# Kernel optimization log

Measured on AMD Instinct MI355X. Metric: run time of the kernel, lower is better.

Reference implementation:

```python
import jax, jax.numpy as jnp
import numpy as np

DIM = 768
NUM_HEADS = 8
HEAD_DIM = DIM // NUM_HEADS


def setup_inputs() -> dict:
    key = jax.random.key(0)
    k1, k2, k3, k4, k5 = jax.random.split(key, 5)
    B, C, H, W = 16, DIM, 32, 32
    x = jax.random.normal(k1, (B, C, H, W), dtype=jnp.float32)
    # Conv2d 1x1 weights expressed as [out_ch, in_ch] matrices
    w_qkv = jax.random.normal(k2, (3 * C, C), dtype=jnp.float32) * (C ** -0.5)
    b_qkv = jax.random.normal(k3, (3 * C,), dtype=jnp.float32) * 0.02
    w_proj = jax.random.normal(k4, (C, C), dtype=jnp.float32) * (C ** -0.5)
    b_proj = jax.random.normal(k5, (C,), dtype=jnp.float32) * 0.02
    return {"x": x, "w_qkv": w_qkv, "b_qkv": b_qkv, "w_proj": w_proj, "b_proj": b_proj}


def reference(x, w_qkv, b_qkv, w_proj, b_proj):
    B, C, H, W = x.shape
    N = H * W
    nh, hd = NUM_HEADS, C // NUM_HEADS
    xf = x.astype(jnp.float32).reshape(B, C, N)  # bcn
    # 1x1 conv == channel matmul
    qkv = jnp.einsum('oc,bcn->bon', w_qkv, xf) + b_qkv[None, :, None]
    qkv = qkv.reshape(B, 3, nh, hd, N)
    q, k, v = qkv[:, 0], qkv[:, 1], qkv[:, 2]  # [B, nh, hd, N]
    s = hd ** -0.25  # scale split between q and k as in the original
    attn = jnp.einsum('bhdn,bhdm->bhnm', q * s, k * s)  # [B, nh, N, N]
    attn = attn - jax.lax.stop_gradient(jnp.max(attn, axis=-1, keepdims=True))
    attn = jnp.clip(attn, -88.0, 88.0)
    attn = jax.nn.softmax(attn, axis=-1)
    # dropout is identity in eval mode
    out = jnp.einsum('bhnm,bhdm->bhdn', attn, v)  # [B, nh, hd, N]
    out = out.reshape(B, C, N)
    out = jnp.einsum('oc,bcn->bon', w_proj, out) + b_proj[None, :, None]
    return out.reshape(B, C, H, W).astype(x.dtype)
```

## Files before the change

### kernel.cpp

```cpp
#include <hip/hip_runtime.h>
#include <stdint.h>

typedef __attribute__((ext_vector_type(4))) float f32x4;
typedef __attribute__((ext_vector_type(16))) float f32x16;
typedef __attribute__((ext_vector_type(8))) short bf16x8;

#define SQKV 0.38372606f
#define RM 8.0f

__device__ __forceinline__ unsigned short f2bf(float f) {
  union { float f; unsigned u; } v; v.f = f;
  unsigned r = v.u + 0x7FFFu + ((v.u >> 16) & 1u);
  return (unsigned short)(r >> 16);
}

__device__ __forceinline__ unsigned cvt_pk_bf16(float a, float b) {
  unsigned r;
  asm volatile("v_cvt_pk_bf16_f32 %0, %1, %2" : "=v"(r) : "v"(a), "v"(b));
  return r;
}
__device__ __forceinline__ void permswap(unsigned &a, unsigned &b) {
  asm volatile("v_permlane32_swap_b32 %0, %1" : "+v"(a), "+v"(b));
}

__device__ __forceinline__ void glds16(const unsigned short* g, unsigned short* l) {
  __builtin_amdgcn_global_load_lds(
      (const __attribute__((address_space(1))) void*)g,
      (__attribute__((address_space(3))) void*)l, 16, 0, 0);
}

__global__ __launch_bounds__(256) void k_convert2(const float* __restrict__ s1,
                                                  const float* __restrict__ s2,
                                                  unsigned short* __restrict__ d1,
                                                  int n1_4, int ntot4) {
  int i = blockIdx.x * 256 + threadIdx.x;
  if (i >= ntot4) return;
  const float4 v = (i < n1_4) ? reinterpret_cast<const float4*>(s1)[i]
                              : reinterpret_cast<const float4*>(s2)[i - n1_4];
  ushort4 o;
  o.x = f2bf(v.x); o.y = f2bf(v.y); o.z = f2bf(v.z); o.w = f2bf(v.w);
  reinterpret_cast<ushort4*>(d1)[i] = o;
}

__global__ __launch_bounds__(256) void k_transpose(const float* __restrict__ x,
                                                   unsigned short* __restrict__ xT) {
  __shared__ float tile[32][33];
  const int t = threadIdx.x;
  const int n0 = blockIdx.x * 32, c0 = blockIdx.y * 32, b = blockIdx.z;
  const int lc = t >> 3, ln = (t & 7) * 4;
  const float4 v = *reinterpret_cast<const float4*>(
      x + ((size_t)b * 768 + c0 + lc) * 1024 + n0 + ln);
  tile[lc][ln] = v.x; tile[lc][ln + 1] = v.y;
  tile[lc][ln + 2] = v.z; tile[lc][ln + 3] = v.w;
  __syncthreads();
  const int sn = t >> 3, sc = (t & 7) * 4;
  ushort4 o;
  o.x = f2bf(tile[sc][sn]);     o.y = f2bf(tile[sc + 1][sn]);
  o.z = f2bf(tile[sc + 2][sn]); o.w = f2bf(tile[sc + 3][sn]);
  *reinterpret_cast<ushort4*>(xT + ((size_t)b * 1024 + n0 + sn) * 768 + c0 + sc) = o;
}

__global__ __launch_bounds__(256, 4) void k_gemm_qkv(
    const unsigned short* __restrict__ A,
    const unsigned short* __restrict__ Bx,
    const float* __restrict__ bias,
    unsigned short* __restrict__ qT,
    unsigned short* __restrict__ kT,
    unsigned short* __restrict__ vO) {
  __shared__ unsigned short As[2 * 128 * 32];
  __shared__ unsigned short Bs[2 * 128 * 32];
  const int t = threadIdx.x;
  const int b = blockIdx.y;
  const int tm = blockIdx.x >> 3, tn = blockIdx.x & 7;
  const int lane = t & 63, w = t >> 6, wr = w >> 1, wc = w & 1;

  const int srow = 16 * w + (lane >> 2);
  const int sg = (lane & 3) ^ ((lane >> 3) & 3);
  const int scol = sg << 3;
  const unsigned short* aptr0 = A + (size_t)(tm * 128 + srow) * 768 + scol;
  const unsigned short* aptr1 = aptr0 + (size_t)64 * 768;
  const unsigned short* bptr0 = Bx + (size_t)b * 1024 * 768 + (size_t)(tn * 128 + srow) * 768 + scol;
  const unsigned short* bptr1 = bptr0 + (size_t)64 * 768;
  unsigned short* const lA0 = As + 512 * w;
  unsigned short* const lA1 = As + 2048 + 512 * w;
  unsigned short* const lB0 = Bs + 512 * w;
  unsigned short* const lB1 = Bs + 2048 + 512 * w;

  f32x4 acc[4][4];
#pragma unroll
  for (int mi = 0; mi < 4; ++mi)
#pragma unroll
    for (int ni = 0; ni < 4; ++ni) acc[mi][ni] = (f32x4)0.0f;

  const int rp = ((lane >> 4) ^ ((lane >> 1) & 3)) << 3;
  const unsigned short* rA[4];
  const unsigned short* rB[4];
#pragma unroll
  for (int mi = 0; mi < 4; ++mi)
    rA[mi] = As + (wr * 64 + mi * 16 + (lane & 15)) * 32 + rp;
#pragma unroll
  for (int ni = 0; ni < 4; ++ni)
    rB[ni] = Bs + (wc * 64 + ni * 16 + (lane & 15)) * 32 + rp;

  glds16(aptr0, lA0);
  glds16(aptr1, lA1);
  glds16(bptr0, lB0);
  glds16(bptr1, lB1);
  aptr0 += 32; aptr1 += 32; bptr0 += 32; bptr1 += 32;

  for (int kt = 0; kt < 24; ++kt) {
    const int cur = kt & 1, nxt = (kt & 1) ^ 1;
    __syncthreads();
    if (kt < 23) {
      glds16(aptr0, lA0 + nxt * 4096);
      glds16(aptr1, lA1 + nxt * 4096);
      glds16(bptr0, lB0 + nxt * 4096);
      glds16(bptr1, lB1 + nxt * 4096);
      aptr0 += 32; aptr1 += 32; bptr0 += 32; bptr1 += 32;
    }

    bf16x8 af[4], bfr[4];
#pragma unroll
    for (int mi = 0; mi < 4; ++mi)
      af[mi] = *reinterpret_cast<const bf16x8*>(rA[mi] + cur * 4096);
#pragma unroll
    for (int ni = 0; ni < 4; ++ni)
      bfr[ni] = *reinterpret_cast<const bf16x8*>(rB[ni] + cur * 4096);
#pragma unroll
    for (int mi = 0; mi < 4; ++mi)
#pragma unroll
      for (int ni = 0; ni < 4; ++ni)
        acc[mi][ni] = __builtin_amdgcn_mfma_f32_16x16x32_bf16(af[mi], bfr[ni], acc[mi][ni], 0, 0, 0);
  }

#pragma unroll
  for (int mi = 0; mi < 4; ++mi) {
    const int o0 = tm * 128 + wr * 64 + mi * 16 + ((lane >> 4) << 2);
    const float4 bb = *reinterpret_cast<const float4*>(bias + o0);
    const float sc = (o0 < 1536) ? SQKV : 1.0f;
    const int om = o0 % 768;
    const int hh = om / 96;
    const int d0 = om % 96;
    const int region = o0 / 768;
    const size_t bh = (size_t)(b * 8 + hh);
#pragma unroll
    for (int ni = 0; ni < 4; ++ni) {
      const int nn = tn * 128 + wc * 64 + ni * 16 + (lane & 15);
      ushort4 st;
      st.x = f2bf((acc[mi][ni][0] + bb.x) * sc);
      st.y = f2bf((acc[mi][ni][1] + bb.y) * sc);
      st.z = f2bf((acc[mi][ni][2] + bb.z) * sc);
      st.w = f2bf((acc[mi][ni][3] + bb.w) * sc);
      if (region == 0) {
        *reinterpret_cast<ushort4*>(qT + (bh * 1024 + nn) * 96 + d0) = st;
      } else if (region == 1) {
        *reinterpret_cast<ushort4*>(kT + (bh * 1024 + nn) * 96 + d0) = st;
      } else {
        unsigned short* vp = vO + (bh * 96 + d0) * 1024 + nn;
        vp[0] = st.x; vp[1024] = st.y; vp[2048] = st.z; vp[3072] = st.w;
      }
    }
  }
}

__global__ __launch_bounds__(512, 2) void k_attn2(
    const unsigned short* __restrict__ qT,
    const unsigned short* __restrict__ kT,
    const unsigned short* __restrict__ vO,
    unsigned short* __restrict__ attoutT) {
  __shared__ unsigned short Ks[2][64 * 104];
  __shared__ unsigned short Vs[2][96 * 72];
  __shared__ float redbuf[8][32];

  const int t = threadIdx.x, lane = t & 63, wv = t >> 6;
  const int r31 = lane & 31, h = lane >> 5;
  const int sw = (blockIdx.x & 7) * 64 + (blockIdx.x >> 3);
  const int bh = sw >> 2, qt = sw & 3;
  const int b = bh >> 3, hh = bh & 7;
  const int n0 = qt * 256 + wv * 32;
  const int off = (blockIdx.x & 1) * 8;

  bf16x8 Qf[6];
  {
    const unsigned short* qrow = qT + ((size_t)bh * 1024 + n0 + r31) * 96 + h * 8;
#pragma unroll
    for (int ks = 0; ks < 6; ++ks)
      Qf[ks] = *reinterpret_cast<const bf16x8*>(qrow + ks * 16);
  }

  const unsigned short* base0[3];
  unsigned short* lptr[3];
  int gstep[3], lstride[3];
#pragma unroll
  for (int i = 0; i < 3; ++i) {
    const int cc = t + i * 512;
    if (cc < 768) {
      const int row = cc / 12, col = (cc % 12) * 8;
      base0[i] = kT + ((size_t)bh * 1024 + row) * 96 + col;
      lptr[i] = &Ks[0][row * 104 + col];
      gstep[i] = 64 * 96;
      lstride[i] = 64 * 104;
    } else {
      const int cv = cc - 768;
      const int d = cv >> 3, col = (cv & 7) * 8;
      base0[i] = vO + ((size_t)bh * 96 + d) * 1024 + col;
      lptr[i] = &Vs[0][d * 72 + col];
      gstep[i] = 64;
      lstride[i] = 96 * 72;
    }
  }
  uint4 rg[3];
#pragma unroll
  for (int i = 0; i < 3; ++i)
    rg[i] = *reinterpret_cast<const uint4*>(base0[i] + (size_t)off * gstep[i]);

  f32x16 oac[3];
#pragma unroll
  for (int dt = 0; dt < 3; ++dt) oac[dt] = (f32x16)0.0f;
  float run_l = 0.0f;

  int cur = 0;
  for (int it = 0; it < 16; ++it, cur ^= 1) {
#pragma unroll
    for (int i = 0; i < 3; ++i)
      *reinterpret_cast<uint4*>(lptr[i] + cur * lstride[i]) = rg[i];
    __syncthreads();
    if (it < 15) {
      const int mtn = (it + 1 + off) & 15;
#pragma unroll
      for (int i = 0; i < 3; ++i)
        rg[i] = *reinterpret_cast<const uint4*>(base0[i] + (size_t)mtn * gstep[i]);
    }
    const unsigned short* Kb = &Ks[cur][0];
    const unsigned short* Vb = &Vs[cur][0];

    f32x16 sa = (f32x16)0.0f, sb = (f32x16)0.0f;
    __builtin_amdgcn_s_setprio(1);
#pragma unroll
    for (int ks = 0; ks < 6; ++ks) {
      const bf16x8 k0 = *reinterpret_cast<const bf16x8*>(Kb + r31 * 104 + ks * 16 + h * 8);
      const bf16x8 k1 = *reinterpret_cast<const bf16x8*>(Kb + (32 + r31) * 104 + ks * 16 + h * 8);
      sa = __builtin_amdgcn_mfma_f32_32x32x16_bf16(k0, Qf[ks], sa, 0, 0, 0);
      sb = __builtin_amdgcn_mfma_f32_32x32x16_bf16(k1, Qf[ks], sb, 0, 0, 0);
    }
    __builtin_amdgcn_s_setprio(0);

    union { bf16x8 v; unsigned u[4]; } pf;

    {
      float t0 = 0.f, t1 = 0.f, t2 = 0.f, t3 = 0.f;
#pragma unroll
      for (int i = 0; i < 16; i += 4) {
        sa[i]     = __builtin_amdgcn_exp2f(sa[i] - RM);     t0 += sa[i];
        sa[i + 1] = __builtin_amdgcn_exp2f(sa[i + 1] - RM); t1 += sa[i + 1];
        sa[i + 2] = __builtin_amdgcn_exp2f(sa[i + 2] - RM); t2 += sa[i + 2];
        sa[i + 3] = __builtin_amdgcn_exp2f(sa[i + 3] - RM); t3 += sa[i + 3];
      }
      float ts = (t0 + t1) + (t2 + t3);
      ts += __shfl_xor(ts, 32);
      run_l += ts;
    }
#pragma unroll
    for (int kst = 0; kst < 2; ++kst) {
      const int base = kst * 8;
      unsigned X = cvt_pk_bf16(sa[base + 0], sa[base + 1]);
      unsigned Y = cvt_pk_bf16(sa[base + 2], sa[base + 3]);
      unsigned Z = cvt_pk_bf16(sa[base + 4], sa[base + 5]);
      unsigned W = cvt_pk_bf16(sa[base + 6], sa[base + 7]);
      permswap(X, Z);
      permswap(Y, W);
      pf.u[0] = X; pf.u[1] = Y; pf.u[2] = Z; pf.u[3] = W;
#pragma unroll
      for (int dt = 0; dt < 3; ++dt) {
        const bf16x8 vf = *reinterpret_cast<const bf16x8*>(
            Vb + (dt * 32 + r31) * 72 + kst * 16 + h * 8);
        oac[dt] = __builtin_amdgcn_mfma_f32_32x32x16_bf16(pf.v, vf, oac[dt], 0, 0, 0);
      }
    }

    {
      float t0 = 0.f, t1 = 0.f, t2 = 0.f, t3 = 0.f;
#pragma unroll
      for (int i = 0; i < 16; i += 4) {
        sb[i]     = __builtin_amdgcn_exp2f(sb[i] - RM);     t0 += sb[i];
        sb[i + 1] = __builtin_amdgcn_exp2f(sb[i + 1] - RM); t1 += sb[i + 1];
        sb[i + 2] = __builtin_amdgcn_exp2f(sb[i + 2] - RM); t2 += sb[i + 2];
        sb[i + 3] = __builtin_amdgcn_exp2f(sb[i + 3] - RM); t3 += sb[i + 3];
      }
      float ts = (t0 + t1) + (t2 + t3);
      ts += __shfl_xor(ts, 32);
      run_l += ts;
    }
#pragma unroll
    for (int kst = 2; kst < 4; ++kst) {
      const int base = (kst & 1) * 8;
      unsigned X = cvt_pk_bf16(sb[base + 0], sb[base + 1]);
      unsigned Y = cvt_pk_bf16(sb[base + 2], sb[base + 3]);
      unsigned Z = cvt_pk_bf16(sb[base + 4], sb[base + 5]);
      unsigned W = cvt_pk_bf16(sb[base + 6], sb[base + 7]);
      permswap(X, Z);
      permswap(Y, W);
      pf.u[0] = X; pf.u[1] = Y; pf.u[2] = Z; pf.u[3] = W;
#pragma unroll
      for (int dt = 0; dt < 3; ++dt) {
        const bf16x8 vf = *reinterpret_cast<const bf16x8*>(
            Vb + (dt * 32 + r31) * 72 + kst * 16 + h * 8);
        oac[dt] = __builtin_amdgcn_mfma_f32_32x32x16_bf16(pf.v, vf, oac[dt], 0, 0, 0);
      }
    }
  }

  if (lane < 32) redbuf[wv][lane] = 1.0f / run_l;
  f32x4 i4[4];
#pragma unroll
  for (int q = 0; q < 4; ++q)
    i4[q] = *reinterpret_cast<const f32x4*>(&redbuf[wv][q * 8 + h * 4]);
  unsigned short* obase = attoutT + ((size_t)b * 1024 + n0) * 768 + hh * 96;
#pragma unroll
  for (int dt = 0; dt < 3; ++dt)
#pragma unroll
    for (int q = 0; q < 4; ++q)
#pragma unroll
      for (int j = 0; j < 4; ++j) {
        const int np = q * 8 + h * 4 + j;
        obase[(size_t)np * 768 + dt * 32 + r31] = f2bf(oac[dt][q * 4 + j] * i4[q][j]);
      }
}

__global__ __launch_bounds__(256, 4) void k_gemm_proj(
    const unsigned short* __restrict__ Aat,
    const unsigned short* __restrict__ Bw,
    const float* __restrict__ bias,
    float* __restrict__ out) {
  __shared__ unsigned short As[2 * 128 * 32];
  __shared__ unsigned short Bs[2 * 128 * 32];
  const int t = threadIdx.x;
  const int b = blockIdx.y;
  const int tm = blockIdx.x / 6, tn = blockIdx.x % 6;
  const int lane = t & 63, w = t >> 6, wr = w >> 1, wc = w & 1;

  const int srow = 16 * w + (lane >> 2);
  const int sg = (lane & 3) ^ ((lane >> 3) & 3);
  const int scol = sg << 3;
  const unsigned short* aptr0 = Aat + (size_t)b * 1024 * 768 + (size_t)(tm * 128 + srow) * 768 + scol;
  const unsigned short* aptr1 = aptr0 + (size_t)64 * 768;
  const unsigned short* bptr0 = Bw + (size_t)(tn * 128 + srow) * 768 + scol;
  const unsigned short* bptr1 = bptr0 + (size_t)64 * 768;
  unsigned short* const lA0 = As + 512 * w;
  unsigned short* const lA1 = As + 2048 + 512 * w;
  unsigned short* const lB0 = Bs + 512 * w;
  unsigned short* const lB1 = Bs + 2048 + 512 * w;

  f32x4 acc[4][4];
#pragma unroll
  for (int mi = 0; mi < 4; ++mi)
#pragma unroll
    for (int ni = 0; ni < 4; ++ni) acc[mi][ni] = (f32x4)0.0f;

  const int rp = ((lane >> 4) ^ ((lane >> 1) & 3)) << 3;
  const unsigned short* rA[4];
  const unsigned short* rB[4];
#pragma unroll
  for (int mi = 0; mi < 4; ++mi)
    rA[mi] = As + (wr * 64 + mi * 16 + (lane & 15)) * 32 + rp;
#pragma unroll
  for (int ni = 0; ni < 4; ++ni)
    rB[ni] = Bs + (wc * 64 + ni * 16 + (lane & 15)) * 32 + rp;

  glds16(aptr0, lA0);
  glds16(aptr1, lA1);
  glds16(bptr0, lB0);
  glds16(bptr1, lB1);
  aptr0 += 32; aptr1 += 32; bptr0 += 32; bptr1 += 32;

  for (int kt = 0; kt < 24; ++kt) {
    const int cur = kt & 1, nxt = (kt & 1) ^ 1;
    __syncthreads();
    if (kt < 23) {
      glds16(aptr0, lA0 + nxt * 4096);
      glds16(aptr1, lA1 + nxt * 4096);
      glds16(bptr0, lB0 + nxt * 4096);
      glds16(bptr1, lB1 + nxt * 4096);
      aptr0 += 32; aptr1 += 32; bptr0 += 32; bptr1 += 32;
    }

    bf16x8 af[4], bfr[4];
#pragma unroll
    for (int mi = 0; mi < 4; ++mi)
      af[mi] = *reinterpret_cast<const bf16x8*>(rA[mi] + cur * 4096);
#pragma unroll
    for (int ni = 0; ni < 4; ++ni)
      bfr[ni] = *reinterpret_cast<const bf16x8*>(rB[ni] + cur * 4096);
#pragma unroll
    for (int mi = 0; mi < 4; ++mi)
#pragma unroll
      for (int ni = 0; ni < 4; ++ni)
        acc[mi][ni] = __builtin_amdgcn_mfma_f32_16x16x32_bf16(af[mi], bfr[ni], acc[mi][ni], 0, 0, 0);
  }

#pragma unroll
  for (int mi = 0; mi < 4; ++mi) {
    const int n0 = tm * 128 + wr * 64 + mi * 16 + ((lane >> 4) << 2);
#pragma unroll
    for (int ni = 0; ni < 4; ++ni) {
      const int o = tn * 128 + wc * 64 + ni * 16 + (lane & 15);
      const float bo = bias[o];
      float4 vv;
      vv.x = acc[mi][ni][0] + bo;
      vv.y = acc[mi][ni][1] + bo;
      vv.z = acc[mi][ni][2] + bo;
      vv.w = acc[mi][ni][3] + bo;
      *reinterpret_cast<float4*>(out + ((size_t)b * 768 + o) * 1024 + n0) = vv;
    }
  }
}

extern "C" void kernel_launch(void* const* d_in, const int* in_sizes, int n_in,
                              void* d_out, int out_size, void* d_ws, size_t ws_size,
                              hipStream_t stream) {
  const float* x = (const float*)d_in[0];
  const float* w_qkv = (const float*)d_in[1];
  const float* b_qkv = (const float*)d_in[2];
  const float* w_proj = (const float*)d_in[3];
  const float* b_proj = (const float*)d_in[4];
  float* out = (float*)d_out;

  unsigned short* ws = (unsigned short*)d_ws;
  unsigned short* wqkv_bf = ws;
  unsigned short* wproj_bf = wqkv_bf + 2304 * 768;
  unsigned short* xT = wproj_bf + 768 * 768;
  unsigned short* qT = xT + (size_t)16 * 1024 * 768;
  unsigned short* kT = qT + (size_t)16 * 8 * 1024 * 96;
  unsigned short* vO = kT + (size_t)16 * 8 * 1024 * 96;
  unsigned short* attoutT = xT;

  const int n1_4 = 2304 * 768 / 4;
  const int ntot4 = n1_4 + 768 * 768 / 4;
  k_convert2<<<(ntot4 + 255) / 256, 256, 0, stream>>>(w_qkv, w_proj, wqkv_bf, n1_4, ntot4);
  k_transpose<<<dim3(32, 24, 16), 256, 0, stream>>>(x, xT);
  k_gemm_qkv<<<dim3(144, 16), 256, 0, stream>>>(wqkv_bf, xT, b_qkv, qT, kT, vO);
  k_attn2<<<512, 512, 0, stream>>>(qT, kT, vO, attoutT);
  k_gemm_proj<<<dim3(48, 16), 256, 0, stream>>>(attoutT, wproj_bf, b_proj, out);
}
```

Measured before the change: 226.7 us.

## Process two 32-query tiles per wave in attention to reuse K/V fragments

The attention kernel now runs 256 threads per block, and each wave handles 64 query rows as two 32-row tiles. Every K and V fragment read from LDS is reused across two MFMAs, which halves the LDS read traffic per unit of matrix work. The per-block key-tile start offset is dropped, so tiles now stream in order. Register pressure roughly doubles because of the extra accumulators and Q fragments, which risks lower occupancy or spills at the stated launch bounds, and fewer waves per block means less latency hiding.

```diff
diff --git a/kernel.cpp b/kernel.cpp
--- a/kernel.cpp
+++ b/kernel.cpp
@@ -163,159 +163,193 @@
   }
 }
 
-__global__ __launch_bounds__(512, 2) void k_attn2(
+__global__ __launch_bounds__(256, 2) void k_attn3(
     const unsigned short* __restrict__ qT,
     const unsigned short* __restrict__ kT,
     const unsigned short* __restrict__ vO,
     unsigned short* __restrict__ attoutT) {
   __shared__ unsigned short Ks[2][64 * 104];
   __shared__ unsigned short Vs[2][96 * 72];
-  __shared__ float redbuf[8][32];
+  __shared__ float redbuf[4][2][32];
 
   const int t = threadIdx.x, lane = t & 63, wv = t >> 6;
   const int r31 = lane & 31, h = lane >> 5;
   const int sw = (blockIdx.x & 7) * 64 + (blockIdx.x >> 3);
   const int bh = sw >> 2, qt = sw & 3;
   const int b = bh >> 3, hh = bh & 7;
-  const int n0 = qt * 256 + wv * 32;
-  const int off = (blockIdx.x & 1) * 8;
-
-  bf16x8 Qf[6];
+  const int n0 = qt * 256 + wv * 64;
+
+  bf16x8 Qf0[6], Qf1[6];
   {
-    const unsigned short* qrow = qT + ((size_t)bh * 1024 + n0 + r31) * 96 + h * 8;
-#pragma unroll
-    for (int ks = 0; ks < 6; ++ks)
-      Qf[ks] = *reinterpret_cast<const bf16x8*>(qrow + ks * 16);
-  }
-
-  const unsigned short* base0[3];
-  unsigned short* lptr[3];
-  int gstep[3], lstride[3];
-#pragma unroll
-  for (int i = 0; i < 3; ++i) {
-    const int cc = t + i * 512;
-    if (cc < 768) {
+    const unsigned short* q0 = qT + ((size_t)bh * 1024 + n0 + r31) * 96 + h * 8;
+    const unsigned short* q1 = q0 + (size_t)32 * 96;
+#pragma unroll
+    for (int ks = 0; ks < 6; ++ks) {
+      Qf0[ks] = *reinterpret_cast<const bf16x8*>(q0 + ks * 16);
+      Qf1[ks] = *reinterpret_cast<const bf16x8*>(q1 + ks * 16);
+    }
+  }
+
+  const unsigned short* gptr[6];
+  unsigned short* lptr[6];
+#pragma unroll
+  for (int i = 0; i < 6; ++i) {
+    if (i < 3) {
+      const int cc = t + i * 256;
       const int row = cc / 12, col = (cc % 12) * 8;
-      base0[i] = kT + ((size_t)bh * 1024 + row) * 96 + col;
+      gptr[i] = kT + ((size_t)bh * 1024 + row) * 96 + col;
       lptr[i] = &Ks[0][row * 104 + col];
-      gstep[i] = 64 * 96;
-      lstride[i] = 64 * 104;
     } else {
-      const int cv = cc - 768;
+      const int cv = t + (i - 3) * 256;
       const int d = cv >> 3, col = (cv & 7) * 8;
-      base0[i] = vO + ((size_t)bh * 96 + d) * 1024 + col;
+      gptr[i] = vO + ((size_t)bh * 96 + d) * 1024 + col;
       lptr[i] = &Vs[0][d * 72 + col];
-      gstep[i] = 64;
-      lstride[i] = 96 * 72;
-    }
-  }
-  uint4 rg[3];
-#pragma unroll
-  for (int i = 0; i < 3; ++i)
-    rg[i] = *reinterpret_cast<const uint4*>(base0[i] + (size_t)off * gstep[i]);
-
-  f32x16 oac[3];
-#pragma unroll
-  for (int dt = 0; dt < 3; ++dt) oac[dt] = (f32x16)0.0f;
-  float run_l = 0.0f;
+    }
+  }
+  uint4 rg[6];
+#pragma unroll
+  for (int i = 0; i < 6; ++i) rg[i] = *reinterpret_cast<const uint4*>(gptr[i]);
+
+  f32x16 oac0[3], oac1[3];
+#pragma unroll
+  for (int dt = 0; dt < 3; ++dt) { oac0[dt] = (f32x16)0.0f; oac1[dt] = (f32x16)0.0f; }
+  float run_l0 = 0.0f, run_l1 = 0.0f;
 
   int cur = 0;
   for (int it = 0; it < 16; ++it, cur ^= 1) {
 #pragma unroll
-    for (int i = 0; i < 3; ++i)
-      *reinterpret_cast<uint4*>(lptr[i] + cur * lstride[i]) = rg[i];
+    for (int i = 0; i < 6; ++i)
+      *reinterpret_cast<uint4*>(lptr[i] + cur * (i < 3 ? 64 * 104 : 96 * 72)) = rg[i];
     __syncthreads();
     if (it < 15) {
-      const int mtn = (it + 1 + off) & 15;
-#pragma unroll
-      for (int i = 0; i < 3; ++i)
-        rg[i] = *reinterpret_cast<const uint4*>(base0[i] + (size_t)mtn * gstep[i]);
+#pragma unroll
+      for (int i = 0; i < 6; ++i) {
+        gptr[i] += (i < 3) ? 64 * 96 : 64;
+        rg[i] = *reinterpret_cast<const uint4*>(gptr[i]);
+      }
     }
     const unsigned short* Kb = &Ks[cur][0];
     const unsigned short* Vb = &Vs[cur][0];
 
-    f32x16 sa = (f32x16)0.0f, sb = (f32x16)0.0f;
-    __builtin_amdgcn_s_setprio(1);
-#pragma unroll
-    for (int ks = 0; ks < 6; ++ks) {
-      const bf16x8 k0 = *reinterpret_cast<const bf16x8*>(Kb + r31 * 104 + ks * 16 + h * 8);
-      const bf16x8 k1 = *reinterpret_cast<const bf16x8*>(Kb + (32 + r31) * 104 + ks * 16 + h * 8);
-      sa = __builtin_amdgcn_mfma_f32_32x32x16_bf16(k0, Qf[ks], sa, 0, 0, 0);
-      sb = __builtin_amdgcn_mfma_f32_32x32x16_bf16(k1, Qf[ks], sb, 0, 0, 0);
-    }
-    __builtin_amdgcn_s_setprio(0);
-
-    union { bf16x8 v; unsigned u[4]; } pf;
+    union { bf16x8 v; unsigned u[4]; } pf0, pf1;
 
     {
-      float t0 = 0.f, t1 = 0.f, t2 = 0.f, t3 = 0.f;
-#pragma unroll
-      for (int i = 0; i < 16; i += 4) {
-        sa[i]     = __builtin_amdgcn_exp2f(sa[i] - RM);     t0 += sa[i];
-        sa[i + 1] = __builtin_amdgcn_exp2f(sa[i + 1] - RM); t1 += sa[i + 1];
-        sa[i + 2] = __builtin_amdgcn_exp2f(sa[i + 2] - RM); t2 += sa[i + 2];
-        sa[i + 3] = __builtin_amdgcn_exp2f(sa[i + 3] - RM); t3 += sa[i + 3];
-      }
-      float ts = (t0 + t1) + (t2 + t3);
+      f32x16 sa0 = (f32x16)0.0f, sa1 = (f32x16)0.0f;
+      __builtin_amdgcn_s_setprio(1);
+#pragma unroll
+      for (int ks = 0; ks < 6; ++ks) {
+        const bf16x8 k0 = *reinterpret_cast<const bf16x8*>(Kb + r31 * 104 + ks * 16 + h * 8);
+        sa0 = __builtin_amdgcn_mfma_f32_32x32x16_bf16(k0, Qf0[ks], sa0, 0, 0, 0);
+        sa1 = __builtin_amdgcn_mfma_f32_32x32x16_bf16(k0, Qf1[ks], sa1, 0, 0, 0);
+      }
+      __builtin_amdgcn_s_setprio(0);
+
+      float t0 = 0.f, t1 = 0.f, u0 = 0.f, u1 = 0.f;
+#pragma unroll
+      for (int i = 0; i < 16; i += 2) {
+        sa0[i]     = __builtin_amdgcn_exp2f(sa0[i] - RM);     t0 += sa0[i];
+        sa0[i + 1] = __builtin_amdgcn_exp2f(sa0[i + 1] - RM); t1 += sa0[i + 1];
+        sa1[i]     = __builtin_amdgcn_exp2f(sa1[i] - RM);     u0 += sa1[i];
+        sa1[i + 1] = __builtin_amdgcn_exp2f(sa1[i + 1] - RM); u1 += sa1[i + 1];
+      }
+      float ts = t0 + t1, us = u0 + u1;
       ts += __shfl_xor(ts, 32);
-      run_l += ts;
-    }
-#pragma unroll
-    for (int kst = 0; kst < 2; ++kst) {
-      const int base = kst * 8;
-      unsigned X = cvt_pk_bf16(sa[base + 0], sa[base + 1]);
-      unsigned Y = cvt_pk_bf16(sa[base + 2], sa[base + 3]);
-      unsigned Z = cvt_pk_bf16(sa[base + 4], sa[base + 5]);
-      unsigned W = cvt_pk_bf16(sa[base + 6], sa[base + 7]);
-      permswap(X, Z);
-      permswap(Y, W);
-      pf.u[0] = X; pf.u[1] = Y; pf.u[2] = Z; pf.u[3] = W;
-#pragma unroll
-      for (int dt = 0; dt < 3; ++dt) {
-        const bf16x8 vf = *reinterpret_cast<const bf16x8*>(
-            Vb + (dt * 32 + r31) * 72 + kst * 16 + h * 8);
-        oac[dt] = __builtin_amdgcn_mfma_f32_32x32x16_bf16(pf.v, vf, oac[dt], 0, 0, 0);
+      us += __shfl_xor(us, 32);
+      run_l0 += ts; run_l1 += us;
+
+#pragma unroll
+      for (int kst = 0; kst < 2; ++kst) {
+        const int base = kst * 8;
+        {
+          unsigned X = cvt_pk_bf16(sa0[base + 0], sa0[base + 1]);
+          unsigned Y = cvt_pk_bf16(sa0[base + 2], sa0[base + 3]);
+          unsigned Z = cvt_pk_bf16(sa0[base + 4], sa0[base + 5]);
+          unsigned W = cvt_pk_bf16(sa0[base + 6], sa0[base + 7]);
+          permswap(X, Z); permswap(Y, W);
+          pf0.u[0] = X; pf0.u[1] = Y; pf0.u[2] = Z; pf0.u[3] = W;
+        }
+        {
+          unsigned X = cvt_pk_bf16(sa1[base + 0], sa1[base + 1]);
+          unsigned Y = cvt_pk_bf16(sa1[base + 2], sa1[base + 3]);
+          unsigned Z = cvt_pk_bf16(sa1[base + 4], sa1[base + 5]);
+          unsigned W = cvt_pk_bf16(sa1[base + 6], sa1[base + 7]);
+          permswap(X, Z); permswap(Y, W);
+          pf1.u[0] = X; pf1.u[1] = Y; pf1.u[2] = Z; pf1.u[3] = W;
+        }
+#pragma unroll
+        for (int dt = 0; dt < 3; ++dt) {
+          const bf16x8 vf = *reinterpret_cast<const bf16x8*>(
+              Vb + (dt * 32 + r31) * 72 + kst * 16 + h * 8);
+          oac0[dt] = __builtin_amdgcn_mfma_f32_32x32x16_bf16(pf0.v, vf, oac0[dt], 0, 0, 0);
+          oac1[dt] = __builtin_amdgcn_mfma_f32_32x32x16_bf16(pf1.v, vf, oac1[dt], 0, 0, 0);
+        }
       }
     }
 
     {
-      float t0 = 0.f, t1 = 0.f, t2 = 0.f, t3 = 0.f;
-#pragma unroll
-      for (int i = 0; i < 16; i += 4) {
-        sb[i]     = __builtin_amdgcn_exp2f(sb[i] - RM);     t0 += sb[i];
-        sb[i + 1] = __builtin_amdgcn_exp2f(sb[i + 1] - RM); t1 += sb[i + 1];
-        sb[i + 2] = __builtin_amdgcn_exp2f(sb[i + 2] - RM); t2 += sb[i + 2];
-        sb[i + 3] = __builtin_amdgcn_exp2f(sb[i + 3] - RM); t3 += sb[i + 3];
-      }
-      float ts = (t0 + t1) + (t2 + t3);
+      f32x16 sb0 = (f32x16)0.0f, sb1 = (f32x16)0.0f;
+      __builtin_amdgcn_s_setprio(1);
+#pragma unroll
+      for (int ks = 0; ks < 6; ++ks) {
+        const bf16x8 k1 = *reinterpret_cast<const bf16x8*>(Kb + (32 + r31) * 104 + ks * 16 + h * 8);
+        sb0 = __builtin_amdgcn_mfma_f32_32x32x16_bf16(k1, Qf0[ks], sb0, 0, 0, 0);
+        sb1 = __builtin_amdgcn_mfma_f32_32x32x16_bf16(k1, Qf1[ks], sb1, 0, 0, 0);
+      }
+      __builtin_amdgcn_s_setprio(0);
+
+      float t0 = 0.f, t1 = 0.f, u0 = 0.f, u1 = 0.f;
+#pragma unroll
+      for (int i = 0; i < 16; i += 2) {
+        sb0[i]     = __builtin_amdgcn_exp2f(sb0[i] - RM);     t0 += sb0[i];
+        sb0[i + 1] = __builtin_amdgcn_exp2f(sb0[i + 1] - RM); t1 += sb0[i + 1];
+        sb1[i]     = __builtin_amdgcn_exp2f(sb1[i] - RM);     u0 += sb1[i];
+        sb1[i + 1] = __builtin_amdgcn_exp2f(sb1[i + 1] - RM); u1 += sb1[i + 1];
+      }
+      float ts = t0 + t1, us = u0 + u1;
       ts += __shfl_xor(ts, 32);
-      run_l += ts;
-    }
-#pragma unroll
-    for (int kst = 2; kst < 4; ++kst) {
-      const int base = (kst & 1) * 8;
-      unsigned X = cvt_pk_bf16(sb[base + 0], sb[base + 1]);
-      unsigned Y = cvt_pk_bf16(sb[base + 2], sb[base + 3]);
-      unsigned Z = cvt_pk_bf16(sb[base + 4], sb[base + 5]);
-      unsigned W = cvt_pk_bf16(sb[base + 6], sb[base + 7]);
-      permswap(X, Z);
-      permswap(Y, W);
-      pf.u[0] = X; pf.u[1] = Y; pf.u[2] = Z; pf.u[3] = W;
-#pragma unroll
-      for (int dt = 0; dt < 3; ++dt) {
-        const bf16x8 vf = *reinterpret_cast<const bf16x8*>(
-            Vb + (dt * 32 + r31) * 72 + kst * 16 + h * 8);
-        oac[dt] = __builtin_amdgcn_mfma_f32_32x32x16_bf16(pf.v, vf, oac[dt], 0, 0, 0);
-      }
-    }
-  }
-
-  if (lane < 32) redbuf[wv][lane] = 1.0f / run_l;
-  f32x4 i4[4];
-#pragma unroll
-  for (int q = 0; q < 4; ++q)
-    i4[q] = *reinterpret_cast<const f32x4*>(&redbuf[wv][q * 8 + h * 4]);
-  unsigned short* obase = attoutT + ((size_t)b * 1024 + n0) * 768 + hh * 96;
+      us += __shfl_xor(us, 32);
+      run_l0 += ts; run_l1 += us;
+
+#pragma unroll
+      for (int kst = 2; kst < 4; ++kst) {
+        const int base = (kst & 1) * 8;
+        {
+          unsigned X = cvt_pk_bf16(sb0[base + 0], sb0[base + 1]);
+          unsigned Y = cvt_pk_bf16(sb0[base + 2], sb0[base + 3]);
+          unsigned Z = cvt_pk_bf16(sb0[base + 4], sb0[base + 5]);
+          unsigned W = cvt_pk_bf16(sb0[base + 6], sb0[base + 7]);
+          permswap(X, Z); permswap(Y, W);
+          pf0.u[0] = X; pf0.u[1] = Y; pf0.u[2] = Z; pf0.u[3] = W;
+        }
+        {
+          unsigned X = cvt_pk_bf16(sb1[base + 0], sb1[base + 1]);
+          unsigned Y = cvt_pk_bf16(sb1[base + 2], sb1[base + 3]);
+          unsigned Z = cvt_pk_bf16(sb1[base + 4], sb1[base + 5]);
+          unsigned W = cvt_pk_bf16(sb1[base + 6], sb1[base + 7]);
+          permswap(X, Z); permswap(Y, W);
+          pf1.u[0] = X; pf1.u[1] = Y; pf1.u[2] = Z; pf1.u[3] = W;
+        }
+#pragma unroll
+        for (int dt = 0; dt < 3; ++dt) {
+          const bf16x8 vf = *reinterpret_cast<const bf16x8*>(
+              Vb + (dt * 32 + r31) * 72 + kst * 16 + h * 8);
+          oac0[dt] = __builtin_amdgcn_mfma_f32_32x32x16_bf16(pf0.v, vf, oac0[dt], 0, 0, 0);
+          oac1[dt] = __builtin_amdgcn_mfma_f32_32x32x16_bf16(pf1.v, vf, oac1[dt], 0, 0, 0);
+        }
+      }
+    }
+  }
+
+  if (lane < 32) redbuf[wv][0][lane] = 1.0f / run_l0;
+  else           redbuf[wv][1][r31]  = 1.0f / run_l1;
+  f32x4 i40[4], i41[4];
+#pragma unroll
+  for (int q = 0; q < 4; ++q) {
+    i40[q] = *reinterpret_cast<const f32x4*>(&redbuf[wv][0][q * 8 + h * 4]);
+    i41[q] = *reinterpret_cast<const f32x4*>(&redbuf[wv][1][q * 8 + h * 4]);
+  }
+  unsigned short* ob0 = attoutT + ((size_t)b * 1024 + n0) * 768 + hh * 96;
+  unsigned short* ob1 = ob0 + (size_t)32 * 768;
 #pragma unroll
   for (int dt = 0; dt < 3; ++dt)
 #pragma unroll
@@ -323,7 +357,8 @@
 #pragma unroll
       for (int j = 0; j < 4; ++j) {
         const int np = q * 8 + h * 4 + j;
-        obase[(size_t)np * 768 + dt * 32 + r31] = f2bf(oac[dt][q * 4 + j] * i4[q][j]);
+        ob0[(size_t)np * 768 + dt * 32 + r31] = f2bf(oac0[dt][q * 4 + j] * i40[q][j]);
+        ob1[(size_t)np * 768 + dt * 32 + r31] = f2bf(oac1[dt][q * 4 + j] * i41[q][j]);
       }
 }
 
@@ -439,6 +474,6 @@
   k_convert2<<<(ntot4 + 255) / 256, 256, 0, stream>>>(w_qkv, w_proj, wqkv_bf, n1_4, ntot4);
   k_transpose<<<dim3(32, 24, 16), 256, 0, stream>>>(x, xT);
   k_gemm_qkv<<<dim3(144, 16), 256, 0, stream>>>(wqkv_bf, xT, b_qkv, qT, kT, vO);
-  k_attn2<<<512, 512, 0, stream>>>(qT, kT, vO, attoutT);
+  k_attn3<<<512, 256, 0, stream>>>(qT, kT, vO, attoutT);
   k_gemm_proj<<<dim3(48, 16), 256, 0, stream>>>(attoutT, wproj_bf, b_proj, out);
 }
```

Result: no change. 226.7 us (-0.0%).
